# Kernel optimization log

Hardware: AMD Instinct MI355X
Metric: run time of the kernel (lower is better)

The kernel has to match this reference:

```python
import jax, jax.numpy as jnp
import numpy as np

N = 100000      # total nodes in batched graph
E = 3200000     # total edges (avg degree 32)
G = 128         # number of graphs in batch
F_IN = 512      # raw node feature dim
NC = 128        # num_classes = projected feature dim (GraphConv layer-0 input)
HID = 256       # hid_channels
OUT = 10        # out_channels
LYR = 3         # args.lyr
EPS = 1e-5      # BatchNorm1d eps


def setup_inputs() -> dict:
    key = jax.random.key(0)
    ks = jax.random.split(key, 20)
    h = jax.random.normal(ks[0], (N, F_IN), dtype=jnp.float32)
    src = jax.random.randint(ks[1], (E,), 0, N, dtype=jnp.int32)
    dst = jax.random.randint(ks[2], (E,), 0, N, dtype=jnp.int32)
    # contiguous sorted graph assignment: every graph non-empty
    graph_ids = (jnp.arange(N, dtype=jnp.int32) * G) // N
    w_init = jax.random.normal(ks[3], (NC, F_IN), dtype=jnp.float32) * 0.05
    inp = dict(h=h, src=src, dst=dst, graph_ids=graph_ids, w_init=w_init)
    dims = [NC, HID, HID]
    for i in range(LYR):
        inp[f"lw{i}"] = jax.random.normal(ks[4 + i], (dims[i], HID), dtype=jnp.float32) * 0.05
        inp[f"lb{i}"] = jnp.zeros((HID,), jnp.float32)
        inp[f"gamma{i}"] = jnp.ones((HID,), jnp.float32)
        inp[f"beta{i}"] = jnp.zeros((HID,), jnp.float32)
    inp["fc_w"] = jax.random.normal(ks[10], (HID, OUT), dtype=jnp.float32) * 0.05
    inp["fc_b"] = jnp.zeros((OUT,), jnp.float32)
    return inp


def _forward(h, src, dst, graph_ids, w_init, layers, fc_w, fc_b):
    # symmetric normalization (DGL GraphConv norm='both')
    ones_e = jnp.ones((E,), h.dtype)
    out_deg = jax.ops.segment_sum(ones_e, src, num_segments=N)
    in_deg = jax.ops.segment_sum(ones_e, dst, num_segments=N)
    norm_src = jnp.where(out_deg > 0, out_deg ** -0.5, 0.0)  # [N]
    norm_dst = jnp.where(in_deg > 0, in_deg ** -0.5, 0.0)    # [N]

    h = h @ w_init.T  # [N, NC]
    for (lw, lb, gamma, beta) in layers:
        # GraphConv: (D_out^-1/2) gather -> scatter-sum -> (D_in^-1/2), then linear
        m = (h * norm_src[:, None])[src]                       # [E, d]
        agg = jax.ops.segment_sum(m, dst, num_segments=N)       # [N, d]
        h = (agg * norm_dst[:, None]) @ lw + lb                 # [N, HID]
        # BatchNorm1d (training-mode batch stats, biased variance) + ReLU
        mu = jnp.mean(h, axis=0)
        var = jnp.mean((h - mu) ** 2, axis=0)
        h = jax.nn.relu((h - mu) * jax.lax.rsqrt(var + EPS) * gamma + beta)
    # dgl.max_nodes: per-graph max over nodes
    hg = jax.ops.segment_max(h, graph_ids, num_segments=G)      # [G, HID]
    return hg @ fc_w + fc_b                                     # [G, OUT]


def reference(h, src, dst, graph_ids, w_init,
              lw0, lb0, gamma0, beta0,
              lw1, lb1, gamma1, beta1,
              lw2, lb2, gamma2, beta2,
              fc_w, fc_b):
    layers = [(lw0, lb0, gamma0, beta0),
              (lw1, lb1, gamma1, beta1),
              (lw2, lb2, gamma2, beta2)]
    return _forward(h, src, dst, graph_ids, w_init, layers, fc_w, fc_b)
```

## Files before the change

kernel.cpp:

```cpp
#include <hip/hip_runtime.h>
#include <hip/hip_bf16.h>

#define N_NODES 100000
#define N_EDGES 3200000
#define N_GRAPHS 128
#define FIN 512
#define NCLS 128
#define HID 256
#define OUT_DIM 10
#define BN_EPS 1e-5f

#define NBUCK 391
#define EPB   ((N_EDGES + NBUCK - 1) / NBUCK)

typedef unsigned short ush;
typedef ush su16x8 __attribute__((ext_vector_type(8)));
typedef ush su16x4 __attribute__((ext_vector_type(4)));
typedef __bf16 bf16x8v __attribute__((ext_vector_type(8)));
typedef float f32x4v __attribute__((ext_vector_type(4)));

__device__ __forceinline__ float bf2f(ush u) {
    union { unsigned int i; float f; } v; v.i = ((unsigned int)u) << 16; return v.f;
}
__device__ __forceinline__ ush f2bf(float f) {
    union { float f; unsigned int i; } v; v.f = f;
    unsigned int r = v.i + 0x7FFFu + ((v.i >> 16) & 1u);
    return (ush)(r >> 16);
}

template <typename T>
__device__ __forceinline__ auto mfma_sel(T a, T b, f32x4v c, int)
    -> decltype(__builtin_amdgcn_mfma_f32_16x16x32_bf16(a, b, c, 0, 0, 0)) {
    return __builtin_amdgcn_mfma_f32_16x16x32_bf16(a, b, c, 0, 0, 0);
}
template <typename T>
__device__ __forceinline__ f32x4v mfma_sel(T a, T b, f32x4v c, long) {
    return __builtin_amdgcn_mfma_f32_16x16x32_bf16(
        __builtin_bit_cast(bf16x8v, a), __builtin_bit_cast(bf16x8v, b), c, 0, 0, 0);
}
__device__ __forceinline__ f32x4v MFMA_BF16(su16x8 a, su16x8 b, f32x4v c) {
    return mfma_sel(a, b, c, 0);
}

__global__ __launch_bounds__(256) void edge_pass1(const int* __restrict__ src,
                                                  const int* __restrict__ dst,
                                                  int* __restrict__ odeg8,
                                                  int* __restrict__ hist) {
    __shared__ int hc[NBUCK];
    int tid = threadIdx.x, blk = blockIdx.x;
    for (int i = tid; i < NBUCK; i += 256) hc[i] = 0;
    __syncthreads();
    int e0 = blk * EPB, e1 = e0 + EPB; if (e1 > N_EDGES) e1 = N_EDGES;
    int c = blk & 7;
    for (int e = e0 + tid; e < e1; e += 256) {
        atomicAdd(&odeg8[(size_t)c * N_NODES + src[e]], 1);
        atomicAdd(&hc[dst[e] >> 8], 1);
    }
    __syncthreads();
    for (int i = tid; i < NBUCK; i += 256) hist[(size_t)blk * NBUCK + i] = hc[i];
}

__global__ void nsrc_kernel(const int* __restrict__ odeg8, float* __restrict__ nsrc) {
    int n = blockIdx.x * 256 + threadIdx.x;
    if (n < N_NODES) {
        int od = 0;
        #pragma unroll
        for (int c = 0; c < 8; c++) od += odeg8[(size_t)c * N_NODES + n];
        nsrc[n] = od > 0 ? rsqrtf((float)od) : 0.f;
    }
}

__global__ __launch_bounds__(512) void bcnt_kernel(const int* __restrict__ hist,
                                                   int* __restrict__ bcnt) {
    __shared__ int ws[8];
    int b = blockIdx.x, tid = threadIdx.x;
    int lane = tid & 63, wid = tid >> 6;
    int v = (tid < NBUCK) ? hist[(size_t)tid * NBUCK + b] : 0;
    #pragma unroll
    for (int off = 32; off > 0; off >>= 1) v += __shfl_down(v, off, 64);
    if (lane == 0) ws[wid] = v;
    __syncthreads();
    if (tid == 0) {
        int s = 0;
        #pragma unroll
        for (int w = 0; w < 8; w++) s += ws[w];
        bcnt[b] = s;
    }
}

__global__ __launch_bounds__(512) void bscan_kernel(const int* __restrict__ bcnt,
                                                    int* __restrict__ bbase) {
    __shared__ int a[512];
    int tid = threadIdx.x;
    int v = (tid < NBUCK) ? bcnt[tid] : 0;
    a[tid] = v;
    __syncthreads();
    for (int s = 1; s < 512; s <<= 1) {
        int y = (tid >= s) ? a[tid - s] : 0;
        __syncthreads();
        a[tid] += y;
        __syncthreads();
    }
    if (tid < NBUCK) bbase[tid] = a[tid] - v;
    if (tid == 0) bbase[NBUCK] = N_EDGES;
}

__global__ __launch_bounds__(512) void boff_kernel(const int* __restrict__ hist,
                                                   const int* __restrict__ bbase,
                                                   int* __restrict__ off) {
    __shared__ int a[512];
    int b = blockIdx.x, tid = threadIdx.x;
    int v = (tid < NBUCK) ? hist[(size_t)tid * NBUCK + b] : 0;
    a[tid] = v;
    __syncthreads();
    for (int s = 1; s < 512; s <<= 1) {
        int y = (tid >= s) ? a[tid - s] : 0;
        __syncthreads();
        a[tid] += y;
        __syncthreads();
    }
    if (tid < NBUCK) off[(size_t)tid * NBUCK + b] = bbase[b] + a[tid] - v;
}

__global__ __launch_bounds__(256) void stage_kernel(const int* __restrict__ src,
                                                    const int* __restrict__ dst,
                                                    const int* __restrict__ off,
                                                    unsigned int* __restrict__ staged) {
    __shared__ int cur[NBUCK];
    int tid = threadIdx.x, blk = blockIdx.x;
    for (int i = tid; i < NBUCK; i += 256) cur[i] = off[(size_t)blk * NBUCK + i];
    __syncthreads();
    int e0 = blk * EPB, e1 = e0 + EPB; if (e1 > N_EDGES) e1 = N_EDGES;
    for (int e = e0 + tid; e < e1; e += 256) {
        int d = dst[e], s = src[e];
        int pos = atomicAdd(&cur[d >> 8], 1);
        staged[pos] = ((unsigned int)(d & 255) << 24) | (unsigned int)s;
    }
}

__global__ __launch_bounds__(256) void csr_kernel(const unsigned int* __restrict__ staged,
                                                  const int* __restrict__ bbase,
                                                  int* __restrict__ roff,
                                                  float* __restrict__ ndst,
                                                  int* __restrict__ csr) {
    __shared__ int cnt[256], pfx[256], cur[256];
    int b = blockIdx.x, tid = threadIdx.x;
    int beg = bbase[b], end = bbase[b + 1];
    int nodeBase = b * 256;
    int nNodes = N_NODES - nodeBase; if (nNodes > 256) nNodes = 256;
    cnt[tid] = 0;
    __syncthreads();
    for (int e = beg + tid; e < end; e += 256) atomicAdd(&cnt[staged[e] >> 24], 1);
    __syncthreads();
    int v = cnt[tid];
    pfx[tid] = v;
    __syncthreads();
    for (int s = 1; s < 256; s <<= 1) {
        int y = (tid >= s) ? pfx[tid - s] : 0;
        __syncthreads();
        pfx[tid] += y;
        __syncthreads();
    }
    int excl = pfx[tid] - v;
    pfx[tid] = excl;
    cur[tid] = 0;
    if (tid < nNodes) {
        int node = nodeBase + tid;
        roff[node] = beg + excl;
        ndst[node] = v > 0 ? rsqrtf((float)v) : 0.f;
    }
    if (b == NBUCK - 1 && tid == 0) roff[N_NODES] = N_EDGES;
    __syncthreads();
    for (int e = beg + tid; e < end; e += 256) {
        unsigned int w = staged[e];
        int dl = w >> 24;
        int pos = beg + pfx[dl] + atomicAdd(&cur[dl], 1);
        csr[pos] = (int)(w & 0xFFFFFFu);
    }
}

__global__ void cvt_weights(const float* __restrict__ w0, const float* __restrict__ l0,
                            const float* __restrict__ l1, const float* __restrict__ l2,
                            ush* __restrict__ wB0, ush* __restrict__ t0,
                            ush* __restrict__ t1, ush* __restrict__ t2) {
    int i = blockIdx.x * 256 + threadIdx.x;
    if (i < NCLS * FIN) { wB0[i] = f2bf(w0[i]); return; }
    i -= NCLS * FIN;
    if (i < HID * NCLS) { int n = i >> 7, k = i & 127; t0[i] = f2bf(l0[k * HID + n]); return; }
    i -= HID * NCLS;
    if (i < HID * HID) { int n = i >> 8, k = i & 255; t1[i] = f2bf(l1[k * HID + n]); return; }
    i -= HID * HID;
    if (i < HID * HID) { int n = i >> 8, k = i & 255; t2[i] = f2bf(l2[k * HID + n]); }
}
#define CVT_TOTAL (NCLS * FIN + HID * NCLS + HID * HID + HID * HID)

template <bool A_F32, bool DO_STATS>
__global__ __launch_bounds__(256) void mfma_gemm(
    const void* __restrict__ Aptr, const ush* __restrict__ BT,
    ush* __restrict__ C, int M, int K, int NN,
    const float* __restrict__ rowscale, const float* __restrict__ bias,
    float* __restrict__ stats)
{
    __shared__ __align__(16) ush As[128][40];
    __shared__ __align__(16) ush Bs[128][40];
    const int bn0 = blockIdx.x * 128;
    const int bm0 = blockIdx.y * 128;
    const int tid = threadIdx.x;
    const int lane = tid & 63;
    const int wv = tid >> 6;
    const int wm = (wv >> 1) * 64;
    const int wn = (wv & 1) * 64;
    const int lm = lane & 15;
    const int lg = lane >> 4;

    f32x4v zero = {0.f, 0.f, 0.f, 0.f};
    f32x4v acc[4][4];
    #pragma unroll
    for (int mi = 0; mi < 4; mi++)
        #pragma unroll
        for (int ni = 0; ni < 4; ni++) acc[mi][ni] = zero;

    for (int k0 = 0; k0 < K; k0 += 32) {
        #pragma unroll
        for (int i = 0; i < 2; i++) {
            int seg = tid + i * 256;
            int n = seg >> 2, kp = seg & 3;
            su16x8 v = *(const su16x8*)&BT[(size_t)(bn0 + n) * K + k0 + kp * 8];
            *(su16x8*)&Bs[n][kp * 8] = v;
        }
        if constexpr (A_F32) {
            const float* Af = (const float*)Aptr;
            #pragma unroll
            for (int i = 0; i < 4; i++) {
                int seg = tid + i * 256;
                int m = seg >> 3, kp = seg & 7;
                int gm = bm0 + m; if (gm >= M) gm = M - 1;
                float4 v = *(const float4*)&Af[(size_t)gm * K + k0 + kp * 4];
                su16x4 o = { f2bf(v.x), f2bf(v.y), f2bf(v.z), f2bf(v.w) };
                *(su16x4*)&As[m][kp * 4] = o;
            }
        } else {
            const ush* Ab = (const ush*)Aptr;
            #pragma unroll
            for (int i = 0; i < 2; i++) {
                int seg = tid + i * 256;
                int m = seg >> 2, kp = seg & 3;
                int gm = bm0 + m; if (gm >= M) gm = M - 1;
                su16x8 v = *(const su16x8*)&Ab[(size_t)gm * K + k0 + kp * 8];
                *(su16x8*)&As[m][kp * 8] = v;
            }
        }
        __syncthreads();
        su16x8 af[4], bfr[4];
        #pragma unroll
        for (int i = 0; i < 4; i++)
            af[i] = *(const su16x8*)&As[wm + i * 16 + lm][lg * 8];
        #pragma unroll
        for (int i = 0; i < 4; i++)
            bfr[i] = *(const su16x8*)&Bs[wn + i * 16 + lm][lg * 8];
        #pragma unroll
        for (int mi = 0; mi < 4; mi++)
            #pragma unroll
            for (int ni = 0; ni < 4; ni++)
                acc[mi][ni] = MFMA_BF16(af[mi], bfr[ni], acc[mi][ni]);
        __syncthreads();
    }

    float s4[4] = {0.f, 0.f, 0.f, 0.f}, q4[4] = {0.f, 0.f, 0.f, 0.f};
    #pragma unroll
    for (int mi = 0; mi < 4; mi++) {
        #pragma unroll
        for (int j = 0; j < 4; j++) {
            int gm = bm0 + wm + mi * 16 + lg * 4 + j;
            bool valid = gm < M;
            float rs = (rowscale && valid) ? rowscale[gm] : 1.f;
            #pragma unroll
            for (int ni = 0; ni < 4; ni++) {
                int gn = bn0 + wn + ni * 16 + lm;
                float v = acc[mi][ni][j] * rs;
                if (bias) v += bias[gn];
                if (valid) {
                    C[(size_t)gm * NN + gn] = f2bf(v);
                    if constexpr (DO_STATS) { s4[ni] += v; q4[ni] += v * v; }
                }
            }
        }
    }
    if constexpr (DO_STATS) {
        #pragma unroll
        for (int ni = 0; ni < 4; ni++) {
            s4[ni] += __shfl_xor(s4[ni], 16); s4[ni] += __shfl_xor(s4[ni], 32);
            q4[ni] += __shfl_xor(q4[ni], 16); q4[ni] += __shfl_xor(q4[ni], 32);
        }
        if (lg == 0) {
            #pragma unroll
            for (int ni = 0; ni < 4; ni++) {
                int gn = bn0 + wn + ni * 16 + lm;
                atomicAdd(&stats[gn], s4[ni]);
                atomicAdd(&stats[HID + gn], q4[ni]);
            }
        }
    }
}

__global__ __launch_bounds__(256) void agg128(const ush* __restrict__ hs,
                                              const int* __restrict__ roff,
                                              const int* __restrict__ csr,
                                              ush* __restrict__ out)
{
    int node = (blockIdx.x * 256 + threadIdx.x) >> 6;
    int lane = threadIdx.x & 63;
    if (node >= N_NODES) return;
    int q = lane >> 4;
    int c0 = (lane & 15) * 8;
    int beg = roff[node], end = roff[node + 1];
    int len = end - beg;
    int s = beg + ((len * q) >> 2);
    int t = beg + ((len * (q + 1)) >> 2);
    float a0[8] = {}, a1[8] = {}, a2[8] = {}, a3[8] = {};
    int e = s;
    for (; e + 3 < t; e += 4) {
        int i0 = csr[e], i1 = csr[e + 1], i2 = csr[e + 2], i3 = csr[e + 3];
        su16x8 v0 = *(const su16x8*)&hs[(size_t)i0 * 128 + c0];
        su16x8 v1 = *(const su16x8*)&hs[(size_t)i1 * 128 + c0];
        su16x8 v2 = *(const su16x8*)&hs[(size_t)i2 * 128 + c0];
        su16x8 v3 = *(const su16x8*)&hs[(size_t)i3 * 128 + c0];
        #pragma unroll
        for (int j = 0; j < 8; j++) {
            a0[j] += bf2f(v0[j]); a1[j] += bf2f(v1[j]);
            a2[j] += bf2f(v2[j]); a3[j] += bf2f(v3[j]);
        }
    }
    for (; e < t; e++) {
        int i0 = csr[e];
        su16x8 v0 = *(const su16x8*)&hs[(size_t)i0 * 128 + c0];
        #pragma unroll
        for (int j = 0; j < 8; j++) a0[j] += bf2f(v0[j]);
    }
    #pragma unroll
    for (int j = 0; j < 8; j++) {
        a0[j] += a1[j] + a2[j] + a3[j];
        a0[j] += __shfl_xor(a0[j], 16);
        a0[j] += __shfl_xor(a0[j], 32);
    }
    if (lane < 16) {
        su16x8 o;
        #pragma unroll
        for (int j = 0; j < 8; j++) o[j] = f2bf(a0[j]);
        __builtin_nontemporal_store(o, (su16x8*)&out[(size_t)node * 128 + c0]);
    }
}

__global__ __launch_bounds__(256) void agg256(const ush* __restrict__ Q,
                                              const int* __restrict__ roff,
                                              const int* __restrict__ csr,
                                              ush* __restrict__ out)
{
    int node = (blockIdx.x * 256 + threadIdx.x) >> 6;
    int lane = threadIdx.x & 63;
    if (node >= N_NODES) return;
    int half = lane >> 5;
    int c0 = (lane & 31) * 8;
    int beg = roff[node], end = roff[node + 1];
    int len = end - beg;
    int s = beg + ((len * half) >> 1);
    int t = beg + ((len * (half + 1)) >> 1);
    float a0[8] = {}, a1[8] = {}, a2[8] = {}, a3[8] = {};
    int e = s;
    for (; e + 3 < t; e += 4) {
        int i0 = csr[e], i1 = csr[e + 1], i2 = csr[e + 2], i3 = csr[e + 3];
        su16x8 v0 = *(const su16x8*)&Q[(size_t)i0 * 256 + c0];
        su16x8 v1 = *(const su16x8*)&Q[(size_t)i1 * 256 + c0];
        su16x8 v2 = *(const su16x8*)&Q[(size_t)i2 * 256 + c0];
        su16x8 v3 = *(const su16x8*)&Q[(size_t)i3 * 256 + c0];
        #pragma unroll
        for (int j = 0; j < 8; j++) {
            a0[j] += bf2f(v0[j]); a1[j] += bf2f(v1[j]);
            a2[j] += bf2f(v2[j]); a3[j] += bf2f(v3[j]);
        }
    }
    for (; e < t; e++) {
        int i0 = csr[e];
        su16x8 v0 = *(const su16x8*)&Q[(size_t)i0 * 256 + c0];
        #pragma unroll
        for (int j = 0; j < 8; j++) a0[j] += bf2f(v0[j]);
    }
    #pragma unroll
    for (int j = 0; j < 8; j++) {
        a0[j] += a1[j] + a2[j] + a3[j];
        a0[j] += __shfl_xor(a0[j], 32);
    }
    if (lane < 32) {
        su16x8 o;
        #pragma unroll
        for (int j = 0; j < 8; j++) o[j] = f2bf(a0[j]);
        __builtin_nontemporal_store(o, (su16x8*)&out[(size_t)node * 256 + c0]);
    }
}

__global__ __launch_bounds__(256) void bnq_kernel(const ush* __restrict__ P,
                                                  const float* __restrict__ stats,
                                                  const float* __restrict__ gamma,
                                                  const float* __restrict__ beta,
                                                  const float* __restrict__ nsrc,
                                                  ush* __restrict__ Q)
{
    __shared__ float sa[HID], sb[HID];
    int tid = threadIdx.x;
    {
        const float inv_n = 1.f / (float)N_NODES;
        float mu = stats[tid] * inv_n;
        float var = fmaf(-mu, mu, stats[HID + tid] * inv_n);
        float a = gamma[tid] * rsqrtf(var + BN_EPS);
        sa[tid] = a;
        sb[tid] = fmaf(-mu, a, beta[tid]);
    }
    __syncthreads();
    const int total = N_NODES * 32;
    for (int idx = blockIdx.x * 256 + tid; idx < total; idx += gridDim.x * 256) {
        int r = idx >> 5, c0 = (idx & 31) * 8;
        su16x8 v = __builtin_nontemporal_load((const su16x8*)&P[(size_t)r * HID + c0]);
        float ns = nsrc[r];
        su16x8 o;
        #pragma unroll
        for (int j = 0; j < 8; j++) {
            float x = fmaxf(fmaf(bf2f(v[j]), sa[c0 + j], sb[c0 + j]), 0.f) * ns;
            o[j] = f2bf(x);
        }
        *(su16x8*)&Q[(size_t)r * HID + c0] = o;
    }
}

__global__ void gstart_kernel(const int* __restrict__ gids, int* __restrict__ gstart) {
    int n = blockIdx.x * 256 + threadIdx.x;
    if (n >= N_NODES) return;
    int g = gids[n];
    int gp = (n == 0) ? -1 : gids[n - 1];
    for (int gg = gp + 1; gg <= g; gg++) gstart[gg] = n;
    if (n == N_NODES - 1) {
        for (int gg = g + 1; gg <= N_GRAPHS; gg++) gstart[gg] = N_NODES;
    }
}

__global__ __launch_bounds__(256) void segmax_ab(const ush* __restrict__ pre,
                                                 const float* __restrict__ stats,
                                                 const float* __restrict__ gamma,
                                                 const float* __restrict__ beta,
                                                 const int* __restrict__ gstart,
                                                 float* __restrict__ hg) {
    int c = threadIdx.x;
    const float inv_n = 1.f / (float)N_NODES;
    float mu = stats[c] * inv_n;
    float var = fmaf(-mu, mu, stats[HID + c] * inv_n);
    float a = gamma[c] * rsqrtf(var + BN_EPS);
    float b = fmaf(-mu, a, beta[c]);
    int g = blockIdx.x;
    int chunk = blockIdx.y;
    int beg = gstart[g], end = gstart[g + 1];
    int len = end - beg;
    int per = (len + 7) >> 3;
    int s = beg + chunk * per;
    int e = s + per; if (e > end) e = end;
    float m0 = 0.f, m1 = 0.f;
    int n = s;
    for (; n + 1 < e; n += 2) {
        m0 = fmaxf(m0, fmaf(bf2f(pre[(size_t)n * HID + c]), a, b));
        m1 = fmaxf(m1, fmaf(bf2f(pre[(size_t)(n + 1) * HID + c]), a, b));
    }
    if (n < e) m0 = fmaxf(m0, fmaf(bf2f(pre[(size_t)n * HID + c]), a, b));
    float m = fmaxf(fmaxf(m0, m1), 0.f);
    atomicMax((int*)&hg[g * HID + c], __float_as_int(m));
}

__global__ void fc_kernel(const float* __restrict__ hg, const float* __restrict__ w,
                          const float* __restrict__ b, float* __restrict__ out) {
    int idx = blockIdx.x * 256 + threadIdx.x;
    if (idx >= N_GRAPHS * OUT_DIM) return;
    int g = idx / OUT_DIM, j = idx % OUT_DIM;
    float s = b[j];
    for (int c = 0; c < HID; c++) s += hg[g * HID + c] * w[c * OUT_DIM + j];
    out[idx] = s;
}

extern "C" void kernel_launch(void* const* d_in, const int* in_sizes, int n_in,
                              void* d_out, int out_size, void* d_ws, size_t ws_size,
                              hipStream_t stream) {
    const float* h      = (const float*)d_in[0];
    const int*   src    = (const int*)d_in[1];
    const int*   dst    = (const int*)d_in[2];
    const int*   gids   = (const int*)d_in[3];
    const float* w_init = (const float*)d_in[4];
    const float* lw[3]    = { (const float*)d_in[5],  (const float*)d_in[9],  (const float*)d_in[13] };
    const float* lb[3]    = { (const float*)d_in[6],  (const float*)d_in[10], (const float*)d_in[14] };
    const float* gamma[3] = { (const float*)d_in[7],  (const float*)d_in[11], (const float*)d_in[15] };
    const float* beta[3]  = { (const float*)d_in[8],  (const float*)d_in[12], (const float*)d_in[16] };
    const float* fc_w = (const float*)d_in[17];
    const float* fc_b = (const float*)d_in[18];
    float* out = (float*)d_out;

    char* ws = (char*)d_ws;
    size_t off_b = 0;
    auto alloc = [&](size_t bytes) { size_t o = off_b; off_b += (bytes + 255) & ~(size_t)255; return o; };
    size_t o_h0s   = alloc((size_t)N_NODES * NCLS * 2);
    size_t o_aggb  = alloc((size_t)N_NODES * HID * 2);
    size_t o_P     = alloc((size_t)N_NODES * HID * 2);
    size_t o_Q     = alloc((size_t)N_NODES * HID * 2);
    size_t o_wB0   = alloc((size_t)NCLS * FIN * 2);
    size_t o_lwT0  = alloc((size_t)HID * NCLS * 2);
    size_t o_lwT1  = alloc((size_t)HID * HID * 2);
    size_t o_lwT2  = alloc((size_t)HID * HID * 2);
    size_t o_nsrc  = alloc((size_t)N_NODES * 4);
    size_t o_ndst  = alloc((size_t)N_NODES * 4);
    size_t o_odeg8 = alloc((size_t)8 * N_NODES * 4);
    size_t o_roff  = alloc((size_t)(N_NODES + 1) * 4);
    size_t o_csr   = alloc((size_t)N_EDGES * 4);
    size_t o_stg   = alloc((size_t)N_EDGES * 4);
    size_t o_hist  = alloc((size_t)NBUCK * NBUCK * 4);
    size_t o_off   = alloc((size_t)NBUCK * NBUCK * 4);
    size_t o_bcnt  = alloc((size_t)(NBUCK + 1) * 4);
    size_t o_bbase = alloc((size_t)(NBUCK + 1) * 4);
    size_t o_stats = alloc((size_t)3 * 2 * HID * 4);
    size_t o_gst   = alloc((size_t)(N_GRAPHS + 1) * 4);
    size_t o_hg    = alloc((size_t)N_GRAPHS * HID * 4);
    if (off_b > ws_size) return;

    ush*   h0s  = (ush*)(ws + o_h0s);
    ush*   aggb = (ush*)(ws + o_aggb);
    ush*   P    = (ush*)(ws + o_P);
    ush*   Q    = (ush*)(ws + o_Q);
    ush*   wB0  = (ush*)(ws + o_wB0);
    ush*   lwT[3] = { (ush*)(ws + o_lwT0), (ush*)(ws + o_lwT1), (ush*)(ws + o_lwT2) };
    float* nsrc = (float*)(ws + o_nsrc);
    float* ndst = (float*)(ws + o_ndst);
    int*   odeg8= (int*)(ws + o_odeg8);
    int*   roff = (int*)(ws + o_roff);
    int*   csr  = (int*)(ws + o_csr);
    unsigned int* stg = (unsigned int*)(ws + o_stg);
    int*   hist = (int*)(ws + o_hist);
    int*   boff = (int*)(ws + o_off);
    int*   bcnt = (int*)(ws + o_bcnt);
    int*   bbase= (int*)(ws + o_bbase);
    float* stats= (float*)(ws + o_stats);
    int*   gst  = (int*)(ws + o_gst);
    float* hg   = (float*)(ws + o_hg);

    const int nb = (N_NODES + 255) / 256;

    hipMemsetAsync(odeg8, 0, (size_t)8 * N_NODES * 4, stream);
    hipMemsetAsync(stats, 0, 3 * 2 * HID * 4, stream);
    hipMemsetAsync(hg, 0, (size_t)N_GRAPHS * HID * 4, stream);

    edge_pass1<<<NBUCK, 256, 0, stream>>>(src, dst, odeg8, hist);
    nsrc_kernel<<<nb, 256, 0, stream>>>(odeg8, nsrc);

    bcnt_kernel<<<NBUCK, 512, 0, stream>>>(hist, bcnt);
    bscan_kernel<<<1, 512, 0, stream>>>(bcnt, bbase);
    boff_kernel<<<NBUCK, 512, 0, stream>>>(hist, bbase, boff);
    stage_kernel<<<NBUCK, 256, 0, stream>>>(src, dst, boff, stg);
    csr_kernel<<<NBUCK, 256, 0, stream>>>(stg, bbase, roff, ndst, csr);

    gstart_kernel<<<nb, 256, 0, stream>>>(gids, gst);

    cvt_weights<<<(CVT_TOTAL + 255) / 256, 256, 0, stream>>>(w_init, lw[0], lw[1], lw[2],
                                                             wB0, lwT[0], lwT[1], lwT[2]);

    const int mblocks = (N_NODES + 127) / 128;
    const int aggblocks = (N_NODES * 64 + 255) / 256;

    {
        dim3 grid(NCLS / 128, mblocks);
        mfma_gemm<true, false><<<grid, 256, 0, stream>>>(h, wB0, h0s, N_NODES, FIN, NCLS,
                                                         nsrc, nullptr, nullptr);
    }

    agg128<<<aggblocks, 256, 0, stream>>>(h0s, roff, csr, aggb);
    {
        dim3 grid(HID / 128, mblocks);
        mfma_gemm<false, true><<<grid, 256, 0, stream>>>(aggb, lwT[0], P, N_NODES, NCLS, HID,
                                                         ndst, lb[0], stats);
    }

    for (int l = 1; l < 3; l++) {
        bnq_kernel<<<1024, 256, 0, stream>>>(P, stats + (l - 1) * 2 * HID,
                                             gamma[l - 1], beta[l - 1], nsrc, Q);
        agg256<<<aggblocks, 256, 0, stream>>>(Q, roff, csr, aggb);
        dim3 grid(HID / 128, mblocks);
        mfma_gemm<false, true><<<grid, 256, 0, stream>>>(aggb, lwT[l], P, N_NODES, HID, HID,
                                                         ndst, lb[l], stats + l * 2 * HID);
    }

    {
        dim3 grid(N_GRAPHS, 8);
        segmax_ab<<<grid, 256, 0, stream>>>(P, stats + 2 * 2 * HID, gamma[2], beta[2], gst, hg);
    }
    fc_kernel<<<(N_GRAPHS * OUT_DIM + 255) / 256, 256, 0, stream>>>(hg, fc_w, fc_b, out);
}
```

Measured before the change: 1.124 ms.

## Merge prep kernels, privatize BN stats atomics, prefetch CSR indices in aggregation

Replaces the three memsets with one zero kernel and merges nsrc, gstart and weight conversion into a single prep kernel. Bucket counts are now accumulated atomically in edge_pass1, which removes the bcnt kernel. BatchNorm statistic atomics are spread over 8 copies to cut contention, and the readers sum those copies. The aggregation loops software-prefetch the next four CSR indices with nontemporal loads, and bf16 conversion switches to the library intrinsic. Together these aim to reduce launch count and atomic contention, at the cost of extra summation in the readers.

```diff
diff --git a/kernel.cpp b/kernel.cpp
--- a/kernel.cpp
+++ b/kernel.cpp
@@ -12,6 +12,7 @@
 
 #define NBUCK 391
 #define EPB   ((N_EDGES + NBUCK - 1) / NBUCK)
+#define STATS_CPY 1536
 
 typedef unsigned short ush;
 typedef ush su16x8 __attribute__((ext_vector_type(8)));
@@ -23,9 +24,8 @@
     union { unsigned int i; float f; } v; v.i = ((unsigned int)u) << 16; return v.f;
 }
 __device__ __forceinline__ ush f2bf(float f) {
-    union { float f; unsigned int i; } v; v.f = f;
-    unsigned int r = v.i + 0x7FFFu + ((v.i >> 16) & 1u);
-    return (ush)(r >> 16);
+    __hip_bfloat16 b = __float2bfloat16(f);
+    return __builtin_bit_cast(ush, b);
 }
 
 template <typename T>
@@ -42,10 +42,20 @@
     return mfma_sel(a, b, c, 0);
 }
 
+__global__ void zero_kernel(int* __restrict__ odeg8, int* __restrict__ bcnt,
+                            float* __restrict__ stats8, float* __restrict__ hg) {
+    int i = blockIdx.x * 256 + threadIdx.x;
+    if (i < 8 * N_NODES) odeg8[i] = 0;
+    if (i <= NBUCK) bcnt[i] = 0;
+    if (i < 8 * STATS_CPY) stats8[i] = 0.f;
+    if (i < N_GRAPHS * HID) hg[i] = 0.f;
+}
+
 __global__ __launch_bounds__(256) void edge_pass1(const int* __restrict__ src,
                                                   const int* __restrict__ dst,
                                                   int* __restrict__ odeg8,
-                                                  int* __restrict__ hist) {
+                                                  int* __restrict__ hist,
+                                                  int* __restrict__ bcnt) {
     __shared__ int hc[NBUCK];
     int tid = threadIdx.x, blk = blockIdx.x;
     for (int i = tid; i < NBUCK; i += 256) hc[i] = 0;
@@ -57,35 +67,42 @@
         atomicAdd(&hc[dst[e] >> 8], 1);
     }
     __syncthreads();
-    for (int i = tid; i < NBUCK; i += 256) hist[(size_t)blk * NBUCK + i] = hc[i];
-}
-
-__global__ void nsrc_kernel(const int* __restrict__ odeg8, float* __restrict__ nsrc) {
-    int n = blockIdx.x * 256 + threadIdx.x;
-    if (n < N_NODES) {
+    for (int i = tid; i < NBUCK; i += 256) {
+        int v = hc[i];
+        hist[(size_t)blk * NBUCK + i] = v;
+        if (v) atomicAdd(&bcnt[i], v);
+    }
+}
+
+#define CVT_TOTAL (NCLS * FIN + HID * NCLS + HID * HID + HID * HID)
+__global__ void misc_prep(const int* __restrict__ odeg8, float* __restrict__ nsrc,
+                          const int* __restrict__ gids, int* __restrict__ gstart,
+                          const float* __restrict__ w0, const float* __restrict__ l0,
+                          const float* __restrict__ l1, const float* __restrict__ l2,
+                          ush* __restrict__ wB0, ush* __restrict__ t0,
+                          ush* __restrict__ t1, ush* __restrict__ t2) {
+    int i = blockIdx.x * 256 + threadIdx.x;
+    if (i < N_NODES) {
         int od = 0;
         #pragma unroll
-        for (int c = 0; c < 8; c++) od += odeg8[(size_t)c * N_NODES + n];
-        nsrc[n] = od > 0 ? rsqrtf((float)od) : 0.f;
-    }
-}
-
-__global__ __launch_bounds__(512) void bcnt_kernel(const int* __restrict__ hist,
-                                                   int* __restrict__ bcnt) {
-    __shared__ int ws[8];
-    int b = blockIdx.x, tid = threadIdx.x;
-    int lane = tid & 63, wid = tid >> 6;
-    int v = (tid < NBUCK) ? hist[(size_t)tid * NBUCK + b] : 0;
-    #pragma unroll
-    for (int off = 32; off > 0; off >>= 1) v += __shfl_down(v, off, 64);
-    if (lane == 0) ws[wid] = v;
-    __syncthreads();
-    if (tid == 0) {
-        int s = 0;
-        #pragma unroll
-        for (int w = 0; w < 8; w++) s += ws[w];
-        bcnt[b] = s;
-    }
+        for (int c = 0; c < 8; c++) od += odeg8[(size_t)c * N_NODES + i];
+        nsrc[i] = od > 0 ? rsqrtf((float)od) : 0.f;
+        int g = gids[i];
+        int gp = (i == 0) ? -1 : gids[i - 1];
+        for (int gg = gp + 1; gg <= g; gg++) gstart[gg] = i;
+        if (i == N_NODES - 1) {
+            for (int gg = g + 1; gg <= N_GRAPHS; gg++) gstart[gg] = N_NODES;
+        }
+        return;
+    }
+    i -= N_NODES;
+    if (i < NCLS * FIN) { wB0[i] = f2bf(w0[i]); return; }
+    i -= NCLS * FIN;
+    if (i < HID * NCLS) { int n = i >> 7, k = i & 127; t0[i] = f2bf(l0[k * HID + n]); return; }
+    i -= HID * NCLS;
+    if (i < HID * HID) { int n = i >> 8, k = i & 255; t1[i] = f2bf(l1[k * HID + n]); return; }
+    i -= HID * HID;
+    if (i < HID * HID) { int n = i >> 8, k = i & 255; t2[i] = f2bf(l2[k * HID + n]); }
 }
 
 __global__ __launch_bounds__(512) void bscan_kernel(const int* __restrict__ bcnt,
@@ -178,21 +195,6 @@
         csr[pos] = (int)(w & 0xFFFFFFu);
     }
 }
-
-__global__ void cvt_weights(const float* __restrict__ w0, const float* __restrict__ l0,
-                            const float* __restrict__ l1, const float* __restrict__ l2,
-                            ush* __restrict__ wB0, ush* __restrict__ t0,
-                            ush* __restrict__ t1, ush* __restrict__ t2) {
-    int i = blockIdx.x * 256 + threadIdx.x;
-    if (i < NCLS * FIN) { wB0[i] = f2bf(w0[i]); return; }
-    i -= NCLS * FIN;
-    if (i < HID * NCLS) { int n = i >> 7, k = i & 127; t0[i] = f2bf(l0[k * HID + n]); return; }
-    i -= HID * NCLS;
-    if (i < HID * HID) { int n = i >> 8, k = i & 255; t1[i] = f2bf(l1[k * HID + n]); return; }
-    i -= HID * HID;
-    if (i < HID * HID) { int n = i >> 8, k = i & 255; t2[i] = f2bf(l2[k * HID + n]); }
-}
-#define CVT_TOTAL (NCLS * FIN + HID * NCLS + HID * HID + HID * HID)
 
 template <bool A_F32, bool DO_STATS>
 __global__ __launch_bounds__(256) void mfma_gemm(
@@ -287,6 +289,7 @@
         }
     }
     if constexpr (DO_STATS) {
+        float* st = stats + ((blockIdx.x + gridDim.x * blockIdx.y) & 7) * STATS_CPY;
         #pragma unroll
         for (int ni = 0; ni < 4; ni++) {
             s4[ni] += __shfl_xor(s4[ni], 16); s4[ni] += __shfl_xor(s4[ni], 32);
@@ -296,8 +299,8 @@
             #pragma unroll
             for (int ni = 0; ni < 4; ni++) {
                 int gn = bn0 + wn + ni * 16 + lm;
-                atomicAdd(&stats[gn], s4[ni]);
-                atomicAdd(&stats[HID + gn], q4[ni]);
+                atomicAdd(&st[gn], s4[ni]);
+                atomicAdd(&st[HID + gn], q4[ni]);
             }
         }
     }
@@ -319,8 +322,28 @@
     int t = beg + ((len * (q + 1)) >> 2);
     float a0[8] = {}, a1[8] = {}, a2[8] = {}, a3[8] = {};
     int e = s;
-    for (; e + 3 < t; e += 4) {
-        int i0 = csr[e], i1 = csr[e + 1], i2 = csr[e + 2], i3 = csr[e + 3];
+    if (t - e >= 4) {
+        int i0 = __builtin_nontemporal_load(&csr[e]);
+        int i1 = __builtin_nontemporal_load(&csr[e + 1]);
+        int i2 = __builtin_nontemporal_load(&csr[e + 2]);
+        int i3 = __builtin_nontemporal_load(&csr[e + 3]);
+        e += 4;
+        for (; e + 3 < t; e += 4) {
+            int j0 = __builtin_nontemporal_load(&csr[e]);
+            int j1 = __builtin_nontemporal_load(&csr[e + 1]);
+            int j2 = __builtin_nontemporal_load(&csr[e + 2]);
+            int j3 = __builtin_nontemporal_load(&csr[e + 3]);
+            su16x8 v0 = *(const su16x8*)&hs[(size_t)i0 * 128 + c0];
+            su16x8 v1 = *(const su16x8*)&hs[(size_t)i1 * 128 + c0];
+            su16x8 v2 = *(const su16x8*)&hs[(size_t)i2 * 128 + c0];
+            su16x8 v3 = *(const su16x8*)&hs[(size_t)i3 * 128 + c0];
+            #pragma unroll
+            for (int j = 0; j < 8; j++) {
+                a0[j] += bf2f(v0[j]); a1[j] += bf2f(v1[j]);
+                a2[j] += bf2f(v2[j]); a3[j] += bf2f(v3[j]);
+            }
+            i0 = j0; i1 = j1; i2 = j2; i3 = j3;
+        }
         su16x8 v0 = *(const su16x8*)&hs[(size_t)i0 * 128 + c0];
         su16x8 v1 = *(const su16x8*)&hs[(size_t)i1 * 128 + c0];
         su16x8 v2 = *(const su16x8*)&hs[(size_t)i2 * 128 + c0];
@@ -332,7 +355,7 @@
         }
     }
     for (; e < t; e++) {
-        int i0 = csr[e];
+        int i0 = __builtin_nontemporal_load(&csr[e]);
         su16x8 v0 = *(const su16x8*)&hs[(size_t)i0 * 128 + c0];
         #pragma unroll
         for (int j = 0; j < 8; j++) a0[j] += bf2f(v0[j]);
@@ -367,8 +390,28 @@
     int t = beg + ((len * (half + 1)) >> 1);
     float a0[8] = {}, a1[8] = {}, a2[8] = {}, a3[8] = {};
     int e = s;
-    for (; e + 3 < t; e += 4) {
-        int i0 = csr[e], i1 = csr[e + 1], i2 = csr[e + 2], i3 = csr[e + 3];
+    if (t - e >= 4) {
+        int i0 = __builtin_nontemporal_load(&csr[e]);
+        int i1 = __builtin_nontemporal_load(&csr[e + 1]);
+        int i2 = __builtin_nontemporal_load(&csr[e + 2]);
+        int i3 = __builtin_nontemporal_load(&csr[e + 3]);
+        e += 4;
+        for (; e + 3 < t; e += 4) {
+            int j0 = __builtin_nontemporal_load(&csr[e]);
+            int j1 = __builtin_nontemporal_load(&csr[e + 1]);
+            int j2 = __builtin_nontemporal_load(&csr[e + 2]);
+            int j3 = __builtin_nontemporal_load(&csr[e + 3]);
+            su16x8 v0 = *(const su16x8*)&Q[(size_t)i0 * 256 + c0];
+            su16x8 v1 = *(const su16x8*)&Q[(size_t)i1 * 256 + c0];
+            su16x8 v2 = *(const su16x8*)&Q[(size_t)i2 * 256 + c0];
+            su16x8 v3 = *(const su16x8*)&Q[(size_t)i3 * 256 + c0];
+            #pragma unroll
+            for (int j = 0; j < 8; j++) {
+                a0[j] += bf2f(v0[j]); a1[j] += bf2f(v1[j]);
+                a2[j] += bf2f(v2[j]); a3[j] += bf2f(v3[j]);
+            }
+            i0 = j0; i1 = j1; i2 = j2; i3 = j3;
+        }
         su16x8 v0 = *(const su16x8*)&Q[(size_t)i0 * 256 + c0];
         su16x8 v1 = *(const su16x8*)&Q[(size_t)i1 * 256 + c0];
         su16x8 v2 = *(const su16x8*)&Q[(size_t)i2 * 256 + c0];
@@ -380,7 +423,7 @@
         }
     }
     for (; e < t; e++) {
-        int i0 = csr[e];
+        int i0 = __builtin_nontemporal_load(&csr[e]);
         su16x8 v0 = *(const su16x8*)&Q[(size_t)i0 * 256 + c0];
         #pragma unroll
         for (int j = 0; j < 8; j++) a0[j] += bf2f(v0[j]);
@@ -408,9 +451,15 @@
     __shared__ float sa[HID], sb[HID];
     int tid = threadIdx.x;
     {
+        float ssum = 0.f, qsum = 0.f;
+        #pragma unroll
+        for (int c8 = 0; c8 < 8; c8++) {
+            ssum += stats[c8 * STATS_CPY + tid];
+            qsum += stats[c8 * STATS_CPY + HID + tid];
+        }
         const float inv_n = 1.f / (float)N_NODES;
-        float mu = stats[tid] * inv_n;
-        float var = fmaf(-mu, mu, stats[HID + tid] * inv_n);
+        float mu = ssum * inv_n;
+        float var = fmaf(-mu, mu, qsum * inv_n);
         float a = gamma[tid] * rsqrtf(var + BN_EPS);
         sa[tid] = a;
         sb[tid] = fmaf(-mu, a, beta[tid]);
@@ -428,17 +477,6 @@
             o[j] = f2bf(x);
         }
         *(su16x8*)&Q[(size_t)r * HID + c0] = o;
-    }
-}
-
-__global__ void gstart_kernel(const int* __restrict__ gids, int* __restrict__ gstart) {
-    int n = blockIdx.x * 256 + threadIdx.x;
-    if (n >= N_NODES) return;
-    int g = gids[n];
-    int gp = (n == 0) ? -1 : gids[n - 1];
-    for (int gg = gp + 1; gg <= g; gg++) gstart[gg] = n;
-    if (n == N_NODES - 1) {
-        for (int gg = g + 1; gg <= N_GRAPHS; gg++) gstart[gg] = N_NODES;
     }
 }
 
@@ -449,9 +487,15 @@
                                                  const int* __restrict__ gstart,
                                                  float* __restrict__ hg) {
     int c = threadIdx.x;
+    float ssum = 0.f, qsum = 0.f;
+    #pragma unroll
+    for (int c8 = 0; c8 < 8; c8++) {
+        ssum += stats[c8 * STATS_CPY + c];
+        qsum += stats[c8 * STATS_CPY + HID + c];
+    }
     const float inv_n = 1.f / (float)N_NODES;
-    float mu = stats[c] * inv_n;
-    float var = fmaf(-mu, mu, stats[HID + c] * inv_n);
+    float mu = ssum * inv_n;
+    float var = fmaf(-mu, mu, qsum * inv_n);
     float a = gamma[c] * rsqrtf(var + BN_EPS);
     float b = fmaf(-mu, a, beta[c]);
     int g = blockIdx.x;
@@ -519,7 +563,7 @@
     size_t o_off   = alloc((size_t)NBUCK * NBUCK * 4);
     size_t o_bcnt  = alloc((size_t)(NBUCK + 1) * 4);
     size_t o_bbase = alloc((size_t)(NBUCK + 1) * 4);
-    size_t o_stats = alloc((size_t)3 * 2 * HID * 4);
+    size_t o_stat8 = alloc((size_t)8 * STATS_CPY * 4);
     size_t o_gst   = alloc((size_t)(N_GRAPHS + 1) * 4);
     size_t o_hg    = alloc((size_t)N_GRAPHS * HID * 4);
     if (off_b > ws_size) return;
@@ -540,30 +584,22 @@
     int*   boff = (int*)(ws + o_off);
     int*   bcnt = (int*)(ws + o_bcnt);
     int*   bbase= (int*)(ws + o_bbase);
-    float* stats= (float*)(ws + o_stats);
+    float* stats8 = (float*)(ws + o_stat8);
     int*   gst  = (int*)(ws + o_gst);
     float* hg   = (float*)(ws + o_hg);
 
-    const int nb = (N_NODES + 255) / 256;
-
-    hipMemsetAsync(odeg8, 0, (size_t)8 * N_NODES * 4, stream);
-    hipMemsetAsync(stats, 0, 3 * 2 * HID * 4, stream);
-    hipMemsetAsync(hg, 0, (size_t)N_GRAPHS * HID * 4, stream);
-
-    edge_pass1<<<NBUCK, 256, 0, stream>>>(src, dst, odeg8, hist);
-    nsrc_kernel<<<nb, 256, 0, stream>>>(odeg8, nsrc);
-
-    bcnt_kernel<<<NBUCK, 512, 0, stream>>>(hist, bcnt);
+    zero_kernel<<<(8 * N_NODES + 255) / 256, 256, 0, stream>>>(odeg8, bcnt, stats8, hg);
+
+    edge_pass1<<<NBUCK, 256, 0, stream>>>(src, dst, odeg8, hist, bcnt);
+
+    misc_prep<<<(N_NODES + CVT_TOTAL + 255) / 256, 256, 0, stream>>>(
+        odeg8, nsrc, gids, gst, w_init, lw[0], lw[1], lw[2], wB0, lwT[0], lwT[1], lwT[2]);
+
     bscan_kernel<<<1, 512, 0, stream>>>(bcnt, bbase);
     boff_kernel<<<NBUCK, 512, 0, stream>>>(hist, bbase, boff);
     stage_kernel<<<NBUCK, 256, 0, stream>>>(src, dst, boff, stg);
     csr_kernel<<<NBUCK, 256, 0, stream>>>(stg, bbase, roff, ndst, csr);
 
-    gstart_kernel<<<nb, 256, 0, stream>>>(gids, gst);
-
-    cvt_weights<<<(CVT_TOTAL + 255) / 256, 256, 0, stream>>>(w_init, lw[0], lw[1], lw[2],
-                                                             wB0, lwT[0], lwT[1], lwT[2]);
-
     const int mblocks = (N_NODES + 127) / 128;
     const int aggblocks = (N_NODES * 64 + 255) / 256;
 
@@ -577,21 +613,21 @@
     {
         dim3 grid(HID / 128, mblocks);
         mfma_gemm<false, true><<<grid, 256, 0, stream>>>(aggb, lwT[0], P, N_NODES, NCLS, HID,
-                                                         ndst, lb[0], stats);
+                                                         ndst, lb[0], stats8 + 0 * 2 * HID);
     }
 
     for (int l = 1; l < 3; l++) {
-        bnq_kernel<<<1024, 256, 0, stream>>>(P, stats + (l - 1) * 2 * HID,
+        bnq_kernel<<<1024, 256, 0, stream>>>(P, stats8 + (l - 1) * 2 * HID,
                                              gamma[l - 1], beta[l - 1], nsrc, Q);
         agg256<<<aggblocks, 256, 0, stream>>>(Q, roff, csr, aggb);
         dim3 grid(HID / 128, mblocks);
         mfma_gemm<false, true><<<grid, 256, 0, stream>>>(aggb, lwT[l], P, N_NODES, HID, HID,
-                                                         ndst, lb[l], stats + l * 2 * HID);
+                                                         ndst, lb[l], stats8 + l * 2 * HID);
     }
 
     {
         dim3 grid(N_GRAPHS, 8);
-        segmax_ab<<<grid, 256, 0, stream>>>(P, stats + 2 * 2 * HID, gamma[2], beta[2], gst, hg);
+        segmax_ab<<<grid, 256, 0, stream>>>(P, stats8 + 2 * 2 * HID, gamma[2], beta[2], gst, hg);
     }
     fc_kernel<<<(N_GRAPHS * OUT_DIM + 255) / 256, 256, 0, stream>>>(hg, fc_w, fc_b, out);
 }
```

After: 1.101 ms. 2.1% less time.
